# Kernel tuning notes

Hardware: AMD Instinct MI355X
Metric: run time of the kernel (lower is better)

The kernel has to match this reference:

```python
import jax, jax.numpy as jnp
import numpy as np

NUM_HEADS = 4
KEY_DIM = 128


def rel_to_abs(rel):
    # rel: [B, heads, L, ww, 2*ww-1] -> [B, heads, L, ww, ww]
    B, heads, L, ww, dim = rel.shape
    flat = rel.reshape(B, heads, L, ww * (2 * ww - 1))[:, :, :, ww - 1:-1]
    return flat.reshape(B, heads, L, ww, 2 * (ww - 1))[..., :ww]


def relative_logits(pos_q, pos_emb_w, pos_emb_h):
    # pos_q: [B, hh, ww, heads, kd]
    # width logits
    q_w = jnp.transpose(pos_q, (0, 3, 1, 2, 4))           # [B, heads, hh, ww, kd]
    rel_w = jnp.einsum('bhxyd,dr->bhxyr', q_w, pos_emb_w)  # [B, heads, hh, ww, 2ww-1]
    rel_w = rel_to_abs(rel_w)                              # [B, heads, hh, ww, ww]
    # height logits
    q_h = jnp.transpose(pos_q, (0, 3, 2, 1, 4))           # [B, heads, ww, hh, kd]
    rel_h = jnp.einsum('bhyxd,dr->bhyxr', q_h, pos_emb_h)  # [B, heads, ww, hh, 2hh-1]
    rel_h = rel_to_abs(rel_h)                              # [B, heads, ww, hh, hh]
    rel_h = jnp.transpose(rel_h, (0, 1, 3, 2, 4))          # [B, heads, hh, ww, hh]
    # broadcast-add: [B, heads, hh, ww, hh, ww]
    return rel_w[:, :, :, :, None, :] + rel_h[:, :, :, :, :, None]


def setup_inputs() -> dict:
    key = jax.random.key(0)
    ks = jax.random.split(key, 7)
    B, H, W, C = 8, 32, 32, 512
    emb = NUM_HEADS * KEY_DIM
    stddev = KEY_DIM ** (-0.5)
    return {
        'x': jax.random.normal(ks[0], (B, H, W, C), jnp.float32),
        'Wq': jax.random.normal(ks[1], (C, emb), jnp.float32) * 0.02,
        'Wk': jax.random.normal(ks[2], (C, emb), jnp.float32) * 0.02,
        'Wv': jax.random.normal(ks[3], (C, emb), jnp.float32) * 0.02,
        'Wo': jax.random.normal(ks[4], (emb, emb), jnp.float32) * 0.02,
        'pos_emb_w': jax.random.normal(ks[5], (KEY_DIM, 2 * W - 1), jnp.float32) * stddev,
        'pos_emb_h': jax.random.normal(ks[6], (KEY_DIM, 2 * H - 1), jnp.float32) * stddev,
    }


def reference(x, Wq, Wk, Wv, Wo, pos_emb_w, pos_emb_h):
    B, hh, ww, C = x.shape
    heads, kd = NUM_HEADS, KEY_DIM
    L = hh * ww
    scale = 1.0 / jnp.sqrt(jnp.asarray(kd, x.dtype))

    q = (x @ Wq) * scale                                    # [B, hh, ww, heads*kd]
    attn_q = q.reshape(B, L, heads, kd).transpose(0, 2, 1, 3)   # [B, heads, L, kd]
    pos_q = q.reshape(B, hh, ww, heads, kd)
    k = (x @ Wk).reshape(B, L, heads, kd).transpose(0, 2, 3, 1)  # [B, heads, kd, L]
    v = (x @ Wv).reshape(B, L, heads, kd).transpose(0, 2, 1, 3)  # [B, heads, L, kd]

    scores = attn_q @ k                                      # [B, heads, L, L]
    pos = relative_logits(pos_q, pos_emb_w, pos_emb_h)        # [B, heads, hh, ww, hh, ww]
    scores = scores + pos.reshape(B, heads, L, L)
    attn = jax.nn.softmax(scores, axis=-1)

    out = attn @ v                                            # [B, heads, L, kd]
    out = out.transpose(0, 2, 1, 3).reshape(B, hh, ww, heads * kd)
    return out @ Wo
```

## Files before the change

kernel.cpp:

```cpp
#include <hip/hip_runtime.h>
#include <math.h>

typedef unsigned short u16;
typedef unsigned int u32;
typedef __bf16 bf16x8 __attribute__((ext_vector_type(8)));
typedef float f32x4 __attribute__((ext_vector_type(4)));

__device__ __forceinline__ u16 f2b(float f) {
  u32 u = __builtin_bit_cast(u32, f);
  u32 r = (u + 0x7FFFu + ((u >> 16) & 1u)) >> 16;
  return (u16)r;
}

__device__ __forceinline__ void glds16(const void* g, void* lds) {
  __builtin_amdgcn_global_load_lds(
      (const __attribute__((address_space(1))) void*)(void*)(const_cast<void*>(g)),
      (__attribute__((address_space(3))) void*)lds, 16, 0, 0);
}


__global__ __launch_bounds__(256) void castx(const float* __restrict__ x, u16* __restrict__ xb) {
  int idx = blockIdx.x * 256 + threadIdx.x;
  float4 v = ((const float4*)x)[idx];
  ushort4 o;
  o.x = f2b(v.x); o.y = f2b(v.y); o.z = f2b(v.z); o.w = f2b(v.w);
  ((ushort4*)xb)[idx] = o;
}

__global__ __launch_bounds__(256) void buildw(const float* __restrict__ Wq, const float* __restrict__ Wk,
                                              const float* __restrict__ Wv, const float* __restrict__ Wo,
                                              u16* __restrict__ WbigT, u16* __restrict__ WoT) {
  const float SCALE = 0.08838834764831845f;
  int row = blockIdx.x;
  int t = threadIdx.x;
  if (row < 512) {
    for (int k = t; k < 512; k += 256) WbigT[row*512 + k] = f2b(Wq[k*512 + row] * SCALE);
  } else if (row < 1024) {
    int n = row - 512;
    for (int k = t; k < 512; k += 256) WbigT[row*512 + k] = f2b(Wk[k*512 + n]);
  } else if (row < 1536) {
    int n = row - 1024;
    for (int k = t; k < 512; k += 256) WbigT[row*512 + k] = f2b(Wv[k*512 + n]);
  } else if (row < 1544) {
    int rr = row - 1536 + 2040;
    for (int k = t; k < 512; k += 256) WbigT[rr*512 + k] = 0;
  } else {
    int n = row - 1544;
    for (int k = t; k < 512; k += 256) WoT[n*512 + k] = f2b(Wo[k*512 + n]);
  }
}

__global__ __launch_bounds__(256) void wpe_kernel(const float* __restrict__ Wq, const float* __restrict__ pew,
                                                  const float* __restrict__ peh, u16* __restrict__ WbigT) {
  int k = blockIdx.x;
  int t = threadIdx.x;
  __shared__ float wrow[512];
  for (int j = t; j < 512; j += 256) wrow[j] = Wq[k*512 + j];
  __syncthreads();
  if (t < 252) {
    int h = t / 63, r = t - h*63;
    float aw = 0.f, ah = 0.f;
    for (int d = 0; d < 128; d++) {
      float qv = wrow[h*128 + d];
      aw += qv * pew[d*63 + r];
      ah += qv * peh[d*63 + r];
    }
    const float SCALE = 0.08838834764831845f;
    WbigT[(size_t)(1536 + t)*512 + k] = f2b(aw * SCALE);
    WbigT[(size_t)(1788 + t)*512 + k] = f2b(ah * SCALE);
  }
}

template<int MODE>
__global__ __launch_bounds__(256) void gemm_bt(
    const u16* __restrict__ A, const u16* __restrict__ Bt,
    float* __restrict__ outF,
    u16* __restrict__ Qb, u16* __restrict__ Kb, u16* __restrict__ Vt,
    float* __restrict__ RELW, float* __restrict__ RELH)
{
  __shared__ char sm[65536];
  const int tid = threadIdx.x;
  const int w = tid >> 6, l = tid & 63, g = l >> 4, c = l & 15;
  const int bm = blockIdx.x, bn = blockIdx.y;
  const int wm = (w >> 1) * 64, wn = (w & 1) * 64;

  f32x4 acc[4][4];
#pragma unroll
  for (int i = 0; i < 4; i++)
#pragma unroll
    for (int j = 0; j < 4; j++) acc[i][j] = f32x4{0.f, 0.f, 0.f, 0.f};

  const char* Ab = (const char*)A;
  const char* Bb = (const char*)Bt;
  const int rsub = l >> 3;
  const int csw = (((l & 7) ^ rsub) << 4);

#define G_STAGE(kb, p)                                                                    \
  {                                                                                       \
    char* As_ = sm + (p)*32768;                                                           \
    char* Bs_ = As_ + 16384;                                                              \
    const int kbyte = (kb) * 128;                                                         \
    _Pragma("unroll")                                                                     \
    for (int t = 0; t < 4; t++) {                                                         \
      const int row = (w*4 + t)*8 + rsub;                                                 \
      glds16(Ab + (size_t)(bm*128 + row) * 1024 + kbyte + csw, As_ + (w*4 + t)*1024);     \
      glds16(Bb + (size_t)(bn*128 + row) * 1024 + kbyte + csw, Bs_ + (w*4 + t)*1024);     \
    }                                                                                     \
  }

  G_STAGE(0, 0);
  G_STAGE(1, 1);

#pragma unroll
  for (int kb = 0; kb < 8; kb++) {
    const int p = kb & 1;
    if (kb < 7) { asm volatile("s_waitcnt vmcnt(8)" ::: "memory"); }
    else        { asm volatile("s_waitcnt vmcnt(0)" ::: "memory"); }
    __builtin_amdgcn_s_barrier();
    const char* As_ = sm + p*32768;
    const char* Bs_ = As_ + 16384;
#pragma unroll
    for (int ks = 0; ks < 2; ks++) {
      const int koff = (ks*64 + g*16) ^ ((c & 7) << 4);
      bf16x8 af[4], bfr[4];
#pragma unroll
      for (int mf = 0; mf < 4; mf++)
        af[mf] = *(const bf16x8*)(As_ + (wm + mf*16 + c)*128 + koff);
#pragma unroll
      for (int nf = 0; nf < 4; nf++)
        bfr[nf] = *(const bf16x8*)(Bs_ + (wn + nf*16 + c)*128 + koff);
#pragma unroll
      for (int mf = 0; mf < 4; mf++)
#pragma unroll
        for (int nf = 0; nf < 4; nf++)
          acc[mf][nf] = __builtin_amdgcn_mfma_f32_16x16x32_bf16(af[mf], bfr[nf], acc[mf][nf], 0, 0, 0);
    }
    __builtin_amdgcn_s_barrier();
    if (kb < 6) G_STAGE(kb + 2, p);
  }

  if (MODE == 0) {
#pragma unroll
    for (int mf = 0; mf < 4; mf++) {
#pragma unroll
      for (int nf = 0; nf < 4; nf++) {
        const int n = bn*128 + wn + nf*16 + c;
#pragma unroll
        for (int r = 0; r < 4; r++) {
          const int m = bm*128 + wm + mf*16 + g*4 + r;
          outF[(size_t)m*512 + n] = acc[mf][nf][r];
        }
      }
    }
  } else if (bn >= 8 && bn < 12) {
    char* T = sm;
#pragma unroll
    for (int mf = 0; mf < 4; mf++) {
#pragma unroll
      for (int nf = 0; nf < 4; nf++) {
        const int d2 = wn + nf*16 + c;
        const int swz = (d2 & 7) << 4;
#pragma unroll
        for (int r = 0; r < 4; r++) {
          const int i = wm + mf*16 + g*4 + r;
          *(u16*)(T + d2*256 + ((i*2) ^ swz)) = f2b(acc[mf][nf][r]);
        }
      }
    }
    __builtin_amdgcn_s_barrier();
    const int b = bm >> 3, h = bn - 8;
#pragma unroll
    for (int it = 0; it < 8; it++) {
      const int L = it*4096 + tid*16;
      const int d2 = L >> 8, kk = L & 255;
      const int swz = (d2 & 7) << 4;
      bf16x8 vv = *(const bf16x8*)(T + d2*256 + (kk ^ swz));
      char* dst = (char*)Vt + ((size_t)((b*4 + h)*128 + d2) * 1024 + (size_t)(bm & 7)*128) * 2 + kk;
      *(bf16x8*)dst = vv;
    }
  } else {
#pragma unroll
    for (int mf = 0; mf < 4; mf++) {
#pragma unroll
      for (int nf = 0; nf < 4; nf++) {
        const int n = bn*128 + wn + nf*16 + c;
#pragma unroll
        for (int r = 0; r < 4; r++) {
          const int m = bm*128 + wm + mf*16 + g*4 + r;
          const int b = m >> 10, i = m & 1023;
          const float v = acc[mf][nf][r];
          if (n < 512) {
            int h = n >> 7, d = n & 127;
            Qb[(size_t)((b*4 + h)*1024 + i)*128 + d] = f2b(v);
          } else if (n < 1024) {
            int h = (n - 512) >> 7, d = n & 127;
            Kb[(size_t)((b*4 + h)*1024 + i)*128 + d] = f2b(v);
          } else if (n >= 1536 && n < 1788) {
            int q = n - 1536, h = q / 63, r2 = q - h*63;
            RELW[(size_t)((b*4 + h)*1024 + i)*64 + r2] = v;
          } else if (n >= 1788 && n < 2040) {
            int q = n - 1788, h = q / 63, r2 = q - h*63;
            RELH[(size_t)((b*4 + h)*1024 + i)*64 + r2] = v;
          }
        }
      }
    }
  }
#undef G_STAGE
}

__global__ __launch_bounds__(256) void attn_fused(
    const u16* __restrict__ Qb, const u16* __restrict__ Kb, const u16* __restrict__ Vt,
    const float* __restrict__ RELW, const float* __restrict__ RELH,
    u16* __restrict__ AO)
{
  __shared__ char sm[73728];
  char* const Pl = sm + 65536;
  const int tid = threadIdx.x;
  const int w = tid >> 6, l = tid & 63, g = l >> 4, c = l & 15;
  const int bh = blockIdx.x, qt = blockIdx.y;
  const int i0 = qt * 64;

  bf16x8 qf[4];
  {
    const char* qbase = (const char*)Qb + (size_t)(bh*1024 + i0 + w*16 + c) * 256;
#pragma unroll
    for (int s = 0; s < 4; s++) qf[s] = *(const bf16x8*)(qbase + s*64 + g*16);
  }

  const int i = i0 + w*16 + c;
  const int xi = i & 31, yi = i >> 5;
  const float* rw = RELW + ((size_t)(bh*1024 + i) << 6);
  const float* rhb = RELH + ((size_t)(bh*1024 + i) << 6) + (31 - yi);
  float xwh[2][4];
#pragma unroll
  for (int e = 0; e < 2; e++)
#pragma unroll
    for (int r = 0; r < 4; r++) xwh[e][r] = rw[e*16 + g*4 + r - xi + 31];

  f32x4 Oacc[8];
#pragma unroll
  for (int fd = 0; fd < 8; fd++) Oacc[fd] = f32x4{0.f, 0.f, 0.f, 0.f};
  float m_q = -INFINITY, l_q = 0.f;

#define A_STAGE(jt, p)                                                                     \
  {                                                                                        \
    char* Kt_ = sm + (p)*32768;                                                            \
    char* Vs_ = Kt_ + 16384;                                                               \
    const int j0b = (jt) * 64;                                                             \
    _Pragma("unroll")                                                                      \
    for (int t = 0; t < 4; t++) {                                                          \
      const int L = (w*4 + t)*1024 + l*16;                                                 \
      const int jr = L >> 8, jb = L & 255;                                                 \
      glds16((const char*)Kb + (size_t)(bh*1024 + j0b + jr) * 256 + (jb ^ ((jr & 7) << 4)),\
             Kt_ + L);                                                                     \
      const int dr = L >> 7, db = L & 127;                                                 \
      glds16((const char*)Vt + (size_t)(bh*128 + dr) * 2048 + j0b*2 + (db ^ ((dr & 7) << 4)),\
             Vs_ + L);                                                                     \
    }                                                                                      \
  }

  A_STAGE(0, 0);
  A_STAGE(1, 1);
  float yh0 = rhb[0], yh1 = rhb[1];

#pragma unroll 2
  for (int jt = 0; jt < 16; jt++) {
    const int p = jt & 1;
    if (jt < 15) { asm volatile("s_waitcnt vmcnt(8)" ::: "memory"); }
    else         { asm volatile("s_waitcnt vmcnt(0)" ::: "memory"); }
    __builtin_amdgcn_s_barrier();

    const char* Kt_ = sm + p*32768;
    const char* Vs_ = Kt_ + 16384;

    f32x4 acc[4];
#pragma unroll
    for (int fn = 0; fn < 4; fn++) acc[fn] = f32x4{0.f, 0.f, 0.f, 0.f};
    __builtin_amdgcn_s_setprio(1);
#pragma unroll
    for (int s = 0; s < 4; s++) {
      const int koff = (s*64 + g*16) ^ ((c & 7) << 4);
#pragma unroll
      for (int fn = 0; fn < 4; fn++) {
        bf16x8 kf = *(const bf16x8*)(Kt_ + (fn*16 + c)*256 + koff);
        acc[fn] = __builtin_amdgcn_mfma_f32_16x16x32_bf16(kf, qf[s], acc[fn], 0, 0, 0);
      }
    }
    __builtin_amdgcn_s_setprio(0);

#pragma unroll
    for (int fn = 0; fn < 4; fn++)
#pragma unroll
      for (int r = 0; r < 4; r++)
        acc[fn][r] += xwh[fn & 1][r] + ((fn >> 1) ? yh1 : yh0);

    float mx = fmaxf(fmaxf(fmaxf(acc[0][0], acc[0][1]), fmaxf(acc[0][2], acc[0][3])),
                     fmaxf(fmaxf(acc[1][0], acc[1][1]), fmaxf(acc[1][2], acc[1][3])));
    mx = fmaxf(mx, fmaxf(fmaxf(fmaxf(acc[2][0], acc[2][1]), fmaxf(acc[2][2], acc[2][3])),
                         fmaxf(fmaxf(acc[3][0], acc[3][1]), fmaxf(acc[3][2], acc[3][3]))));
    mx = fmaxf(mx, __shfl_xor(mx, 16));
    mx = fmaxf(mx, __shfl_xor(mx, 32));
    const float mnew = fmaxf(m_q, mx);
    const float scq = __expf(m_q - mnew);
    m_q = mnew;

    float pv[4][4];
    float ps = 0.f;
#pragma unroll
    for (int fn = 0; fn < 4; fn++) {
#pragma unroll
      for (int r = 0; r < 4; r++) {
        pv[fn][r] = __expf(acc[fn][r] - mnew);
        ps += pv[fn][r];
      }
    }
    ps += __shfl_xor(ps, 16);
    ps += __shfl_xor(ps, 32);
    l_q = l_q * scq + ps;

    float nyh0 = 0.f, nyh1 = 0.f;
    if (jt < 15) { nyh0 = rhb[(jt + 1)*2]; nyh1 = rhb[(jt + 1)*2 + 1]; }

    {
      char* pb = Pl + w*2048 + c*128;
      const int swz = (c & 7) << 4;
#pragma unroll
      for (int fn = 0; fn < 4; fn++) {
        u32 w0, w1;
        asm("v_cvt_pk_bf16_f32 %0, %1, %2" : "=v"(w0) : "v"(pv[fn][0]), "v"(pv[fn][1]));
        asm("v_cvt_pk_bf16_f32 %0, %1, %2" : "=v"(w1) : "v"(pv[fn][2]), "v"(pv[fn][3]));
        uint2 pk; pk.x = w0; pk.y = w1;
        *(uint2*)(pb + ((fn*32 + g*8) ^ swz)) = pk;
      }
    }

#pragma unroll
    for (int r = 0; r < 4; r++) {
      const float scr = __shfl(scq, g*4 + r, 16);
#pragma unroll
      for (int fd = 0; fd < 8; fd++) Oacc[fd][r] *= scr;
    }

    __builtin_amdgcn_s_setprio(1);
#pragma unroll
    for (int s = 0; s < 2; s++) {
      const int koff = (s*64 + g*16) ^ ((c & 7) << 4);
      bf16x8 pf = *(const bf16x8*)(Pl + w*2048 + c*128 + koff);
#pragma unroll
      for (int fd = 0; fd < 8; fd++) {
        bf16x8 vf = *(const bf16x8*)(Vs_ + (fd*16 + c)*128 + koff);
        Oacc[fd] = __builtin_amdgcn_mfma_f32_16x16x32_bf16(pf, vf, Oacc[fd], 0, 0, 0);
      }
    }
    __builtin_amdgcn_s_setprio(0);

    __builtin_amdgcn_s_barrier();
    if (jt < 14) A_STAGE(jt + 2, p);
    yh0 = nyh0; yh1 = nyh1;
  }

  const int b = bh >> 2, h = bh & 3;
#pragma unroll
  for (int r = 0; r < 4; r++) {
    const float lr = __shfl(l_q, g*4 + r, 16);
    const float linv = 1.0f / lr;
    const int io = i0 + w*16 + g*4 + r;
#pragma unroll
    for (int fd = 0; fd < 8; fd++) {
      AO[(size_t)(b*1024 + io)*512 + h*128 + fd*16 + c] = f2b(Oacc[fd][r] * linv);
    }
  }
#undef A_STAGE
}

extern "C" void kernel_launch(void* const* d_in, const int* in_sizes, int n_in,
                              void* d_out, int out_size, void* d_ws, size_t ws_size,
                              hipStream_t stream) {
  const float* x   = (const float*)d_in[0];
  const float* Wq  = (const float*)d_in[1];
  const float* Wk  = (const float*)d_in[2];
  const float* Wv  = (const float*)d_in[3];
  const float* Wo  = (const float*)d_in[4];
  const float* pew = (const float*)d_in[5];
  const float* peh = (const float*)d_in[6];

  char* ws = (char*)d_ws;
  u16* xb    = (u16*)ws;    ws += (size_t)8192*512*2;
  u16* WbigT = (u16*)ws;    ws += (size_t)2048*512*2;
  u16* WoT   = (u16*)ws;    ws += (size_t)512*512*2;
  u16* Qb    = (u16*)ws;    ws += (size_t)32*1024*128*2;
  u16* Kb    = (u16*)ws;    ws += (size_t)32*1024*128*2;
  u16* Vt    = (u16*)ws;    ws += (size_t)32*1024*128*2;
  float* RELW = (float*)ws; ws += (size_t)32*1024*64*4;
  float* RELH = (float*)ws; ws += (size_t)32*1024*64*4;
  u16* AO    = (u16*)ws;    ws += (size_t)8192*512*2;

  castx<<<4096, 256, 0, stream>>>(x, xb);
  buildw<<<2056, 256, 0, stream>>>(Wq, Wk, Wv, Wo, WbigT, WoT);
  wpe_kernel<<<512, 256, 0, stream>>>(Wq, pew, peh, WbigT);
  gemm_bt<1><<<dim3(64, 16), 256, 0, stream>>>(xb, WbigT, nullptr, Qb, Kb, Vt, RELW, RELH);
  attn_fused<<<dim3(32, 16), 256, 0, stream>>>(Qb, Kb, Vt, RELW, RELH, AO);
  gemm_bt<0><<<dim3(64, 4), 256, 0, stream>>>(AO, WoT, (float*)d_out,
                                              nullptr, nullptr, nullptr, nullptr, nullptr);
}
```

Measured before the change: 104.5 us.

## Use 256x256-tile projection GEMM with LDS-staged coalesced Q/K/V epilogue

Replaces the 128x128-tile QKV/positional projection GEMM with a 512-thread kernel using 256x256 tiles, 128KB double-buffered LDS, and 8x4 MFMA fragments per wave, which halves the grid and raises operand reuse. Q and K outputs now go through a swizzled LDS transpose and are written as 16-byte vectors instead of scattered 2-byte stores. V is packed with v_cvt_pk_bf16_f32 before its transpose. The larger tile cuts occupancy to one block per CU and leaves only 256 blocks, and some tiles in the rel-logit column range are partly idle.

```diff
diff --git a/kernel.cpp b/kernel.cpp
--- a/kernel.cpp
+++ b/kernel.cpp
@@ -71,12 +71,152 @@
   }
 }
 
-template<int MODE>
-__global__ __launch_bounds__(256) void gemm_bt(
+__global__ __launch_bounds__(512) void gemm256(
     const u16* __restrict__ A, const u16* __restrict__ Bt,
-    float* __restrict__ outF,
     u16* __restrict__ Qb, u16* __restrict__ Kb, u16* __restrict__ Vt,
     float* __restrict__ RELW, float* __restrict__ RELH)
+{
+  __shared__ char sm[131072];
+  const int tid = threadIdx.x;
+  const int w = tid >> 6, l = tid & 63, g = l >> 4, c = l & 15;
+  const int bm = blockIdx.x, bn = blockIdx.y;
+  const int wm = w >> 2, wn = w & 3;
+
+  f32x4 acc[8][4];
+#pragma unroll
+  for (int i = 0; i < 8; i++)
+#pragma unroll
+    for (int j = 0; j < 4; j++) acc[i][j] = f32x4{0.f, 0.f, 0.f, 0.f};
+
+  const char* Ab = (const char*)A;
+  const char* Bb = (const char*)Bt;
+  const int rsub = l >> 3;
+  const int csw = (((l & 7) ^ rsub) << 4);
+
+#define G_STAGE(kb, p)                                                                    \
+  {                                                                                       \
+    char* As_ = sm + (p)*65536;                                                           \
+    char* Bs_ = As_ + 32768;                                                              \
+    const int kbyte = (kb) * 128;                                                         \
+    _Pragma("unroll")                                                                     \
+    for (int i2 = 0; i2 < 4; i2++) {                                                      \
+      const int row = i2*64 + w*8 + rsub;                                                 \
+      glds16(Ab + (size_t)(bm*256 + row) * 1024 + kbyte + csw, As_ + i2*8192 + w*1024);   \
+      glds16(Bb + (size_t)(bn*256 + row) * 1024 + kbyte + csw, Bs_ + i2*8192 + w*1024);   \
+    }                                                                                     \
+  }
+
+  G_STAGE(0, 0);
+  G_STAGE(1, 1);
+
+#pragma unroll
+  for (int kb = 0; kb < 8; kb++) {
+    const int p = kb & 1;
+    if (kb < 7) { asm volatile("s_waitcnt vmcnt(8)" ::: "memory"); }
+    else        { asm volatile("s_waitcnt vmcnt(0)" ::: "memory"); }
+    __builtin_amdgcn_s_barrier();
+    const char* As_ = sm + p*65536;
+    const char* Bs_ = As_ + 32768;
+#pragma unroll
+    for (int ks = 0; ks < 2; ks++) {
+      const int koff = (ks*64 + g*16) ^ ((c & 7) << 4);
+      bf16x8 af[8], bfr[4];
+#pragma unroll
+      for (int mf = 0; mf < 8; mf++)
+        af[mf] = *(const bf16x8*)(As_ + (wm*128 + mf*16 + c)*128 + koff);
+#pragma unroll
+      for (int nf = 0; nf < 4; nf++)
+        bfr[nf] = *(const bf16x8*)(Bs_ + (wn*64 + nf*16 + c)*128 + koff);
+#pragma unroll
+      for (int mf = 0; mf < 8; mf++)
+#pragma unroll
+        for (int nf = 0; nf < 4; nf++)
+          acc[mf][nf] = __builtin_amdgcn_mfma_f32_16x16x32_bf16(af[mf], bfr[nf], acc[mf][nf], 0, 0, 0);
+    }
+    __builtin_amdgcn_s_barrier();
+    if (kb < 6) G_STAGE(kb + 2, p);
+  }
+#undef G_STAGE
+
+  const int b = bm >> 2;
+  const int iBase = (bm & 3) * 256;
+
+  if (bn < 4) {
+    u16* dst0 = (bn < 2) ? Qb : Kb;
+    const int bnn = bn & 1;
+#pragma unroll
+    for (int mf = 0; mf < 8; mf++) {
+      const int lmb = wm*128 + mf*16 + g*4;
+#pragma unroll
+      for (int nf = 0; nf < 4; nf++) {
+        const int ln = wn*64 + nf*16 + c;
+#pragma unroll
+        for (int r = 0; r < 4; r++) {
+          const int lm = lmb + r;
+          *(u16*)(sm + lm*512 + ((ln*2) ^ ((lm & 7) << 4))) = f2b(acc[mf][nf][r]);
+        }
+      }
+    }
+    __builtin_amdgcn_s_barrier();
+#pragma unroll
+    for (int it = 0; it < 16; it++) {
+      const int gid = it*512 + tid;
+      const int lm2 = gid >> 5, gsub = gid & 31;
+      bf16x8 v = *(const bf16x8*)(sm + lm2*512 + ((gsub*16) ^ ((lm2 & 7) << 4)));
+      const int h = bnn*2 + (gsub >> 4);
+      const int d0 = (gsub & 15) * 8;
+      *(bf16x8*)(dst0 + ((size_t)(b*4 + h)*1024 + iBase + lm2)*128 + d0) = v;
+    }
+  } else if (bn < 6) {
+#pragma unroll
+    for (int mf = 0; mf < 8; mf++) {
+      const int lmb = wm*128 + mf*16 + g*4;
+#pragma unroll
+      for (int nf = 0; nf < 4; nf++) {
+        const int ln = wn*64 + nf*16 + c;
+        u32 w0, w1;
+        asm("v_cvt_pk_bf16_f32 %0, %1, %2" : "=v"(w0) : "v"(acc[mf][nf][0]), "v"(acc[mf][nf][1]));
+        asm("v_cvt_pk_bf16_f32 %0, %1, %2" : "=v"(w1) : "v"(acc[mf][nf][2]), "v"(acc[mf][nf][3]));
+        uint2 pk; pk.x = w0; pk.y = w1;
+        *(uint2*)(sm + ln*512 + ((lmb*2) ^ ((c & 7) << 4))) = pk;
+      }
+    }
+    __builtin_amdgcn_s_barrier();
+#pragma unroll
+    for (int it = 0; it < 16; it++) {
+      const int gid = it*512 + tid;
+      const int ln2 = gid >> 5, gsub = gid & 31;
+      bf16x8 v = *(const bf16x8*)(sm + ln2*512 + ((gsub*16) ^ ((ln2 & 7) << 4)));
+      const int q2 = (bn - 4)*256 + ln2;
+      const int h = q2 >> 7, d = q2 & 127;
+      *(bf16x8*)(Vt + ((size_t)(b*4 + h)*128 + d)*1024 + iBase + gsub*8) = v;
+    }
+  } else {
+#pragma unroll
+    for (int mf = 0; mf < 8; mf++) {
+      const int lmb = wm*128 + mf*16 + g*4;
+#pragma unroll
+      for (int nf = 0; nf < 4; nf++) {
+        const int q = (bn - 6)*256 + wn*64 + nf*16 + c;
+        if (q < 252) {
+          const int h = q / 63, r2 = q - h*63;
+#pragma unroll
+          for (int r = 0; r < 4; r++)
+            RELW[(size_t)((b*4 + h)*1024 + iBase + lmb + r)*64 + r2] = acc[mf][nf][r];
+        } else if (q < 504) {
+          const int qq = q - 252;
+          const int h = qq / 63, r2 = qq - h*63;
+#pragma unroll
+          for (int r = 0; r < 4; r++)
+            RELH[(size_t)((b*4 + h)*1024 + iBase + lmb + r)*64 + r2] = acc[mf][nf][r];
+        }
+      }
+    }
+  }
+}
+
+__global__ __launch_bounds__(256) void gemm_out(
+    const u16* __restrict__ A, const u16* __restrict__ Bt, float* __restrict__ outF)
 {
   __shared__ char sm[65536];
   const int tid = threadIdx.x;
@@ -138,75 +278,20 @@
     __builtin_amdgcn_s_barrier();
     if (kb < 6) G_STAGE(kb + 2, p);
   }
-
-  if (MODE == 0) {
-#pragma unroll
-    for (int mf = 0; mf < 4; mf++) {
-#pragma unroll
-      for (int nf = 0; nf < 4; nf++) {
-        const int n = bn*128 + wn + nf*16 + c;
-#pragma unroll
-        for (int r = 0; r < 4; r++) {
-          const int m = bm*128 + wm + mf*16 + g*4 + r;
-          outF[(size_t)m*512 + n] = acc[mf][nf][r];
-        }
-      }
-    }
-  } else if (bn >= 8 && bn < 12) {
-    char* T = sm;
-#pragma unroll
-    for (int mf = 0; mf < 4; mf++) {
-#pragma unroll
-      for (int nf = 0; nf < 4; nf++) {
-        const int d2 = wn + nf*16 + c;
-        const int swz = (d2 & 7) << 4;
-#pragma unroll
-        for (int r = 0; r < 4; r++) {
-          const int i = wm + mf*16 + g*4 + r;
-          *(u16*)(T + d2*256 + ((i*2) ^ swz)) = f2b(acc[mf][nf][r]);
-        }
-      }
-    }
-    __builtin_amdgcn_s_barrier();
-    const int b = bm >> 3, h = bn - 8;
-#pragma unroll
-    for (int it = 0; it < 8; it++) {
-      const int L = it*4096 + tid*16;
-      const int d2 = L >> 8, kk = L & 255;
-      const int swz = (d2 & 7) << 4;
-      bf16x8 vv = *(const bf16x8*)(T + d2*256 + (kk ^ swz));
-      char* dst = (char*)Vt + ((size_t)((b*4 + h)*128 + d2) * 1024 + (size_t)(bm & 7)*128) * 2 + kk;
-      *(bf16x8*)dst = vv;
-    }
-  } else {
-#pragma unroll
-    for (int mf = 0; mf < 4; mf++) {
-#pragma unroll
-      for (int nf = 0; nf < 4; nf++) {
-        const int n = bn*128 + wn + nf*16 + c;
-#pragma unroll
-        for (int r = 0; r < 4; r++) {
-          const int m = bm*128 + wm + mf*16 + g*4 + r;
-          const int b = m >> 10, i = m & 1023;
-          const float v = acc[mf][nf][r];
-          if (n < 512) {
-            int h = n >> 7, d = n & 127;
-            Qb[(size_t)((b*4 + h)*1024 + i)*128 + d] = f2b(v);
-          } else if (n < 1024) {
-            int h = (n - 512) >> 7, d = n & 127;
-            Kb[(size_t)((b*4 + h)*1024 + i)*128 + d] = f2b(v);
-          } else if (n >= 1536 && n < 1788) {
-            int q = n - 1536, h = q / 63, r2 = q - h*63;
-            RELW[(size_t)((b*4 + h)*1024 + i)*64 + r2] = v;
-          } else if (n >= 1788 && n < 2040) {
-            int q = n - 1788, h = q / 63, r2 = q - h*63;
-            RELH[(size_t)((b*4 + h)*1024 + i)*64 + r2] = v;
-          }
-        }
-      }
-    }
-  }
 #undef G_STAGE
+
+#pragma unroll
+  for (int mf = 0; mf < 4; mf++) {
+#pragma unroll
+    for (int nf = 0; nf < 4; nf++) {
+      const int n = bn*128 + wn + nf*16 + c;
+#pragma unroll
+      for (int r = 0; r < 4; r++) {
+        const int m = bm*128 + wm + mf*16 + g*4 + r;
+        outF[(size_t)m*512 + n] = acc[mf][nf][r];
+      }
+    }
+  }
 }
 
 __global__ __launch_bounds__(256) void attn_fused(
@@ -399,8 +484,7 @@
   castx<<<4096, 256, 0, stream>>>(x, xb);
   buildw<<<2056, 256, 0, stream>>>(Wq, Wk, Wv, Wo, WbigT, WoT);
   wpe_kernel<<<512, 256, 0, stream>>>(Wq, pew, peh, WbigT);
-  gemm_bt<1><<<dim3(64, 16), 256, 0, stream>>>(xb, WbigT, nullptr, Qb, Kb, Vt, RELW, RELH);
+  gemm256<<<dim3(32, 8), 512, 0, stream>>>(xb, WbigT, Qb, Kb, Vt, RELW, RELH);
   attn_fused<<<dim3(32, 16), 256, 0, stream>>>(Qb, Kb, Vt, RELW, RELH, AO);
-  gemm_bt<0><<<dim3(64, 4), 256, 0, stream>>>(AO, WoT, (float*)d_out,
-                                              nullptr, nullptr, nullptr, nullptr, nullptr);
-}
+  gemm_out<<<dim3(64, 4), 256, 0, stream>>>(AO, WoT, (float*)d_out);
+}
```

Measured after the change: 97.63 us. 1.07x faster.
